# Kernel optimization log

Hardware: AMD Instinct MI355X
Metric: run time of the kernel (lower is better)

## Reference

```python
import jax, jax.numpy as jnp
import numpy as np

H, W, C = 64, 64, 64
B = 64
N_HEADS = 4
CONV_FILTERS = 64
BASIS_DIM = 16


def get_spatial_basis(h, w, d):
    half_d = d // 2
    basis = np.zeros((h, w, d), dtype=np.float32)
    div = np.exp(np.arange(0, half_d, 2, dtype=np.float32) * -np.log(100.0) / half_d)
    h_grid = np.expand_dims(np.arange(0, h, dtype=np.float32), 1)
    w_grid = np.expand_dims(np.arange(0, w, dtype=np.float32), 1)
    basis[:, :, 0:half_d:2] = np.sin(h_grid * div)[:, np.newaxis, :]
    basis[:, :, 1:half_d:2] = np.cos(h_grid * div)[:, np.newaxis, :]
    basis[:, :, half_d::2] = np.sin(w_grid * div)[np.newaxis, :, :]
    basis[:, :, half_d + 1::2] = np.cos(w_grid * div)[np.newaxis, :, :]
    return basis


def setup_inputs() -> dict:
    key = jax.random.key(0)
    ks = jax.random.split(key, 8)
    feat_in = C + BASIS_DIM  # 80 input channels for 1x1 convs
    return {
        "image": jax.random.normal(ks[0], (B, H, W, C), jnp.float32),
        "state1": jax.random.normal(ks[1], (B, 512), jnp.float32),
        "state2": jax.random.normal(ks[2], (B, 512), jnp.float32),
        "extra": jax.random.normal(ks[3], (B, 256), jnp.float32),
        "Wq": jax.random.normal(ks[4], (1024, CONV_FILTERS), jnp.float32) * 0.03,
        "bq": jnp.zeros((CONV_FILTERS,), jnp.float32),
        "Wk": jax.random.normal(ks[5], (feat_in, CONV_FILTERS), jnp.float32) * 0.1,
        "bk": jnp.zeros((CONV_FILTERS,), jnp.float32),
        "Wv": jax.random.normal(ks[6], (feat_in, CONV_FILTERS), jnp.float32) * 0.1,
        "bv": jnp.zeros((CONV_FILTERS,), jnp.float32),
        "spatial_basis": jnp.asarray(get_spatial_basis(H, W, BASIS_DIM)),
    }


def reference(image, state1, state2, extra, Wq, bq, Wk, bk, Wv, bv, spatial_basis):
    b, h, w, _ = image.shape
    nh = N_HEADS
    cf = Wq.shape[1]
    dph = cf // nh  # depth per head

    # concat image with tiled spatial basis -> [B,h,w,C+basis_dim]
    sb = jnp.broadcast_to(spatial_basis[None], (b,) + spatial_basis.shape)
    feats = jnp.concatenate([image, sb], axis=-1)

    # combiner over network-state tensors, then Dense query
    state = jnp.concatenate([state1, state2], axis=-1)  # [B,1024]
    q = state @ Wq + bq                                 # [B,cf]

    # 1x1 convs == per-pixel dense projections
    keys = feats @ Wk + bk    # [B,h,w,cf]
    vals = feats @ Wv + bv    # [B,h,w,cf]

    qh = q.reshape(b, nh, dph)
    kh = keys.reshape(b, h * w, nh, dph)
    vh = vals.reshape(b, h * w, nh, dph)

    # per-head dot scores over spatial positions, softmax over positions
    scores = jnp.einsum('bnd,bpnd->bpn', qh, kh)        # [B,hw,nh]
    attn = jax.nn.softmax(scores, axis=1)
    mean_attn = attn.mean(axis=-1).reshape(b, h, w)

    # weighted sum of values over spatial positions -> [B,cf]
    pooled = jnp.einsum('bpn,bpnd->bnd', attn, vh).reshape(b, cf)

    out = jnp.concatenate([pooled, extra], axis=-1)
    return out, mean_attn
```

## Files before the change

kernel.cpp:

```cpp
#include <hip/hip_runtime.h>
#include <hip/hip_bf16.h>

#define BATCH  64
#define HW     4096
#define PTILE  256
#define NSPLIT 16
#define RSTRIDE 88

typedef unsigned int u32;
typedef unsigned short u16;

__device__ __forceinline__ float bf2f(u16 h) { return __uint_as_float(((u32)h) << 16); }

__device__ __forceinline__ u32 f2bf(float x) {
  u32 b = __float_as_uint(x);
  return (b + 0x7fffu + ((b >> 16) & 1u)) >> 16;
}

template<bool F32>
__device__ __forceinline__ float ld(const void* p, size_t i) {
  if (F32) return ((const float*)p)[i];
  return bf2f(((const u16*)p)[i]);
}

template<bool F32>
__device__ __forceinline__ void st(void* p, size_t i, float v) {
  if (F32) ((float*)p)[i] = v;
  else     ((__hip_bfloat16*)p)[i] = __float2bfloat16(v);
}

__device__ __forceinline__ bool detect_f32(const u16* __restrict__ image) {
  u16 h = image[(threadIdx.x & 63) * 2];
  u32 e = (h >> 7) & 0xFFu;
  unsigned long long m = __ballot(e >= 0x86u);
  return __popcll(m) >= 8;
}

__device__ __forceinline__ void acc8(uint4 v, const float* __restrict__ w,
                                     float& s0, float& s1, float& s2, float& s3) {
  const u32 uu[4] = {v.x, v.y, v.z, v.w};
#pragma unroll
  for (int i = 0; i < 4; ++i) {
    float lo = __uint_as_float(uu[i] << 16);
    float hi = __uint_as_float(uu[i] & 0xffff0000u);
    const float* wl = w + i * 8;
    s0 += lo * wl[0]; s1 += lo * wl[1]; s2 += lo * wl[2]; s3 += lo * wl[3];
    s0 += hi * wl[4]; s1 += hi * wl[5]; s2 += hi * wl[6]; s3 += hi * wl[7];
  }
}

template<bool F32>
__device__ void k1_body(const void* state1, const void* state2, const void* Wq,
                        const void* bq, const void* Wk, const void* bk,
                        float* weff, float* cb, float* stt, float* qp, float* q) {
  const int b = blockIdx.x, tid = threadIdx.x;
  stt[tid]        = ld<F32>(state1, (size_t)b * 512 + tid);
  stt[512 + tid]  = ld<F32>(state2, (size_t)b * 512 + tid);
  __syncthreads();
  {
    const int j = tid & 63, k = tid >> 6, i0 = k * 128;
    float a = 0.f;
    for (int i = 0; i < 128; ++i) a += stt[i0 + i] * ld<F32>(Wq, (size_t)(i0 + i) * 64 + j);
    qp[k * 64 + j] = a;
  }
  __syncthreads();
  if (tid < 64) {
    float a = ld<F32>(bq, tid);
#pragma unroll
    for (int k = 0; k < 8; ++k) a += qp[k * 64 + tid];
    q[tid] = a;
  }
  __syncthreads();
  if (tid < 320) {
    const int c = tid >> 2, n = tid & 3;
    float a = 0.f;
#pragma unroll
    for (int d = 0; d < 16; ++d) a += ld<F32>(Wk, (size_t)c * 64 + n * 16 + d) * q[n * 16 + d];
    weff[b * 320 + tid] = a;
  } else if (tid < 324) {
    const int n = tid - 320;
    float a = 0.f;
#pragma unroll
    for (int d = 0; d < 16; ++d) a += ld<F32>(bk, n * 16 + d) * q[n * 16 + d];
    cb[b * 4 + n] = a;
  }
}

__global__ __launch_bounds__(512) void k1_prep(
    const void* image, const void* state1, const void* state2, const void* Wq,
    const void* bq, const void* Wk, const void* bk, float* weff, float* cb) {
  __shared__ float stt[1024];
  __shared__ float qp[512];
  __shared__ float q[64];
  if (detect_f32((const u16*)image))
       k1_body<true >(state1, state2, Wq, bq, Wk, bk, weff, cb, stt, qp, q);
  else k1_body<false>(state1, state2, Wq, bq, Wk, bk, weff, cb, stt, qp, q);
}

__global__ __launch_bounds__(256) void k2_main(
    const void* __restrict__ image, const void* __restrict__ basis,
    const float* __restrict__ weff, const float* __restrict__ cb,
    float* __restrict__ e_buf, float* __restrict__ m_blk, float* __restrict__ sum_blk,
    float* __restrict__ fpool_part) {
  __shared__ __align__(16) u16 feat[PTILE * RSTRIDE];
  __shared__ __align__(16) float es_t[4 * PTILE];
  __shared__ float red[16];
  __shared__ float bm[4];
  const int tid = threadIdx.x;
  const int b = blockIdx.x & 63, s = blockIdx.x >> 6;
  const int bs = b * NSPLIT + s;

  if (detect_f32((const u16*)image)) {
    const float4* img4 = (const float4*)image + ((size_t)b * HW + s * PTILE) * 16;
#pragma unroll
    for (int i = 0; i < 16; ++i) {
      const int f = i * 256 + tid;
      float4 v = img4[f];
      const int r = f >> 4, c4 = f & 15;
      u32 lo = f2bf(v.x) | (f2bf(v.y) << 16);
      u32 hi = f2bf(v.z) | (f2bf(v.w) << 16);
      *(uint2*)(feat + r * RSTRIDE + c4 * 4) = make_uint2(lo, hi);
    }
    const float4* bas4 = (const float4*)basis + (size_t)(s * PTILE) * 4;
#pragma unroll
    for (int i = 0; i < 4; ++i) {
      const int f = i * 256 + tid;
      float4 v = bas4[f];
      const int r = f >> 2, c4 = f & 3;
      u32 lo = f2bf(v.x) | (f2bf(v.y) << 16);
      u32 hi = f2bf(v.z) | (f2bf(v.w) << 16);
      *(uint2*)(feat + r * RSTRIDE + 64 + c4 * 4) = make_uint2(lo, hi);
    }
  } else {
    const uint4* img4 = (const uint4*)image + ((size_t)b * HW + s * PTILE) * 8;
#pragma unroll
    for (int i = 0; i < 8; ++i) {
      const int f = i * 256 + tid;
      const int r = f >> 3, c8 = f & 7;
      *(uint4*)(feat + r * RSTRIDE + c8 * 8) = img4[f];
    }
    const uint4* bas4 = (const uint4*)basis + (size_t)(s * PTILE) * 2;
#pragma unroll
    for (int i = 0; i < 2; ++i) {
      const int f = i * 256 + tid;
      const int r = f >> 1, c8 = f & 1;
      *(uint4*)(feat + r * RSTRIDE + 64 + c8 * 8) = bas4[f];
    }
  }
  __syncthreads();

  const float* wf = weff + b * 320;
  float s0 = cb[b * 4 + 0], s1 = cb[b * 4 + 1], s2 = cb[b * 4 + 2], s3 = cb[b * 4 + 3];
  {
    const uint4* row = (const uint4*)(feat + tid * RSTRIDE);
#pragma unroll
    for (int v = 0; v < 10; ++v) acc8(row[v], wf + v * 32, s0, s1, s2, s3);
  }

  float m0 = s0, m1 = s1, m2 = s2, m3 = s3;
#pragma unroll
  for (int off = 32; off > 0; off >>= 1) {
    m0 = fmaxf(m0, __shfl_xor(m0, off, 64));
    m1 = fmaxf(m1, __shfl_xor(m1, off, 64));
    m2 = fmaxf(m2, __shfl_xor(m2, off, 64));
    m3 = fmaxf(m3, __shfl_xor(m3, off, 64));
  }
  if ((tid & 63) == 0) { float* r = red + (tid >> 6) * 4; r[0] = m0; r[1] = m1; r[2] = m2; r[3] = m3; }
  __syncthreads();
  if (tid < 4) {
    float m = red[tid];
#pragma unroll
    for (int w = 1; w < 4; ++w) m = fmaxf(m, red[w * 4 + tid]);
    bm[tid] = m;
  }
  __syncthreads();

  float e0 = __expf(s0 - bm[0]);
  float e1 = __expf(s1 - bm[1]);
  float e2 = __expf(s2 - bm[2]);
  float e3 = __expf(s3 - bm[3]);
  es_t[0 * PTILE + tid] = e0;
  es_t[1 * PTILE + tid] = e1;
  es_t[2 * PTILE + tid] = e2;
  es_t[3 * PTILE + tid] = e3;
  reinterpret_cast<float4*>(e_buf)[(size_t)b * HW + s * PTILE + tid] = make_float4(e0, e1, e2, e3);

  float a0 = e0, a1 = e1, a2 = e2, a3 = e3;
#pragma unroll
  for (int off = 32; off > 0; off >>= 1) {
    a0 += __shfl_xor(a0, off, 64);
    a1 += __shfl_xor(a1, off, 64);
    a2 += __shfl_xor(a2, off, 64);
    a3 += __shfl_xor(a3, off, 64);
  }
  if ((tid & 63) == 0) { float* r = red + (tid >> 6) * 4; r[0] = a0; r[1] = a1; r[2] = a2; r[3] = a3; }
  __syncthreads();
  if (tid < 4) {
    float a = 0.f;
#pragma unroll
    for (int w = 0; w < 4; ++w) a += red[w * 4 + tid];
    sum_blk[bs * 4 + tid] = a;
    m_blk[bs * 4 + tid] = bm[tid];
  }

  {
    const int n = tid >> 6, c = tid & 63;
    const float4* esn = (const float4*)(es_t + n * PTILE);
    float acc = 0.f, acc2 = 0.f;
#pragma unroll 8
    for (int g = 0; g < 64; ++g) {
      float4 e = esn[g];
      const u16* f0 = feat + (g * 4) * RSTRIDE + c;
      acc += e.x * bf2f(f0[0]) + e.y * bf2f(f0[RSTRIDE]) +
             e.z * bf2f(f0[2 * RSTRIDE]) + e.w * bf2f(f0[3 * RSTRIDE]);
      if (c < 16) {
        const u16* f1 = f0 + 64;
        acc2 += e.x * bf2f(f1[0]) + e.y * bf2f(f1[RSTRIDE]) +
                e.z * bf2f(f1[2 * RSTRIDE]) + e.w * bf2f(f1[3 * RSTRIDE]);
      }
    }
    fpool_part[(size_t)bs * 320 + n * 80 + c] = acc;
    if (c < 16) fpool_part[(size_t)bs * 320 + n * 80 + 64 + c] = acc2;
  }
}

template<bool F32>
__device__ void k34_body(const float* m_blk, const float* sum_blk, const float* e_buf,
                         const float* fpool_part, const void* Wv, const void* bv,
                         const void* extra, void* out, float* esc, float* fp) {
  const int tid = threadIdx.x;
  const int b = blockIdx.x & 63, s = blockIdx.x >> 6;
  if (tid < 4) {
    float M = -3.4e38f;
#pragma unroll
    for (int sp = 0; sp < NSPLIT; ++sp) M = fmaxf(M, m_blk[(b * NSPLIT + sp) * 4 + tid]);
    float den = 0.f;
#pragma unroll
    for (int sp = 0; sp < NSPLIT; ++sp)
      den += __expf(m_blk[(b * NSPLIT + sp) * 4 + tid] - M) * sum_blk[(b * NSPLIT + sp) * 4 + tid];
    float rd = 1.0f / den;
#pragma unroll
    for (int sp = 0; sp < NSPLIT; ++sp)
      esc[sp * 4 + tid] = __expf(m_blk[(b * NSPLIT + sp) * 4 + tid] - M) * rd;
  }
  __syncthreads();
  {
    float4 e4 = reinterpret_cast<const float4*>(e_buf)[(size_t)b * HW + s * PTILE + tid];
    float mean = 0.25f * (e4.x * esc[s * 4 + 0] + e4.y * esc[s * 4 + 1] +
                          e4.z * esc[s * 4 + 2] + e4.w * esc[s * 4 + 3]);
    st<F32>(out, (size_t)BATCH * 320 + (size_t)b * HW + s * PTILE + tid, mean);
  }
  if (s == 0) {
    for (int idx = tid; idx < 320; idx += 256) {
      const int n2 = idx / 80;
      float a = 0.f;
#pragma unroll
      for (int sp = 0; sp < NSPLIT; ++sp)
        a += esc[sp * 4 + n2] * fpool_part[(size_t)(b * NSPLIT + sp) * 320 + idx];
      fp[idx] = a;
    }
    __syncthreads();
    if (tid < 64) {
      const int n = tid >> 4;
      float dot = 0.f;
#pragma unroll
      for (int c = 0; c < 80; ++c) dot += fp[n * 80 + c] * ld<F32>(Wv, (size_t)c * 64 + tid);
      st<F32>(out, (size_t)b * 320 + tid, dot + ld<F32>(bv, tid));
    }
    st<F32>(out, (size_t)b * 320 + 64 + tid, ld<F32>(extra, (size_t)b * 256 + tid));
  }
}

__global__ __launch_bounds__(256) void k34_out(
    const void* image, const float* m_blk, const float* sum_blk, const float* e_buf,
    const float* fpool_part, const void* Wv, const void* bv, const void* extra, void* out) {
  __shared__ float esc[NSPLIT * 4];
  __shared__ float fp[320];
  if (detect_f32((const u16*)image))
       k34_body<true >(m_blk, sum_blk, e_buf, fpool_part, Wv, bv, extra, out, esc, fp);
  else k34_body<false>(m_blk, sum_blk, e_buf, fpool_part, Wv, bv, extra, out, esc, fp);
}

extern "C" void kernel_launch(void* const* d_in, const int* in_sizes, int n_in,
                              void* d_out, int out_size, void* d_ws, size_t ws_size,
                              hipStream_t stream) {
  (void)in_sizes; (void)n_in; (void)out_size; (void)ws_size;
  const void* image  = d_in[0];
  const void* state1 = d_in[1];
  const void* state2 = d_in[2];
  const void* extra  = d_in[3];
  const void* Wq = d_in[4];
  const void* bq = d_in[5];
  const void* Wk = d_in[6];
  const void* bk = d_in[7];
  const void* Wv = d_in[8];
  const void* bv = d_in[9];
  const void* basis = d_in[10];

  float* ws         = (float*)d_ws;
  float* weff       = ws;
  float* cb         = ws + 20480;
  float* m_blk      = ws + 20736;
  float* sum_blk    = ws + 24832;
  float* fpool_part = ws + 28928;
  float* e_buf      = ws + 356608;

  k1_prep<<<dim3(BATCH), dim3(512), 0, stream>>>(image, state1, state2, Wq, bq, Wk, bk, weff, cb);
  k2_main<<<dim3(BATCH * NSPLIT), dim3(PTILE), 0, stream>>>(image, basis, weff, cb,
                                                            e_buf, m_blk, sum_blk, fpool_part);
  k34_out<<<dim3(BATCH * NSPLIT), dim3(PTILE), 0, stream>>>(image, m_blk, sum_blk, e_buf,
                                                            fpool_part, Wv, bv, extra, d_out);
}
```

Baseline: 144.2 us.

## Split query GEMM across batch tiles and transpose feature tile to channel-major

The query projection becomes a separate 16-block kernel that tiles Wq and states in shared memory and reuses each weight across 16 batch rows, followed by a small reduction kernel that forms the effective key weights. The main kernel stores the feature tile channel-major in LDS so both the score dot product and the pooled-value accumulation read contiguous 16-byte vectors. Scores are computed by 8 threads per group of 8 pixels, then reduced with lane shuffles. The e_buf layout changes to head-major. This adds an extra kernel launch and a redundant LDS load left over in the score loop.

```diff
diff --git a/kernel.cpp b/kernel.cpp
--- a/kernel.cpp
+++ b/kernel.cpp
@@ -5,7 +5,7 @@
 #define HW     4096
 #define PTILE  256
 #define NSPLIT 16
-#define RSTRIDE 88
+#define RST    264
 
 typedef unsigned int u32;
 typedef unsigned short u16;
@@ -21,6 +21,13 @@
 __device__ __forceinline__ float ld(const void* p, size_t i) {
   if (F32) return ((const float*)p)[i];
   return bf2f(((const u16*)p)[i]);
+}
+
+template<bool F32>
+__device__ __forceinline__ float4 ld4(const void* p, size_t i4) {
+  if (F32) return ((const float4*)p)[i4];
+  uint2 u = ((const uint2*)p)[i4];
+  return make_float4(bf2f(u.x & 0xffff), bf2f(u.x >> 16), bf2f(u.y & 0xffff), bf2f(u.y >> 16));
 }
 
 template<bool F32>
@@ -36,38 +43,65 @@
   return __popcll(m) >= 8;
 }
 
-__device__ __forceinline__ void acc8(uint4 v, const float* __restrict__ w,
-                                     float& s0, float& s1, float& s2, float& s3) {
-  const u32 uu[4] = {v.x, v.y, v.z, v.w};
+template<bool F32>
+__device__ void k1a_body(const void* state1, const void* state2, const void* Wq,
+                         float* q_part, float* WslT, float* stt) {
+  const int kb = blockIdx.x;
+  const int tid = threadIdx.x;
 #pragma unroll
   for (int i = 0; i < 4; ++i) {
-    float lo = __uint_as_float(uu[i] << 16);
-    float hi = __uint_as_float(uu[i] & 0xffff0000u);
-    const float* wl = w + i * 8;
-    s0 += lo * wl[0]; s1 += lo * wl[1]; s2 += lo * wl[2]; s3 += lo * wl[3];
-    s0 += hi * wl[4]; s1 += hi * wl[5]; s2 += hi * wl[6]; s3 += hi * wl[7];
-  }
-}
-
-template<bool F32>
-__device__ void k1_body(const void* state1, const void* state2, const void* Wq,
-                        const void* bq, const void* Wk, const void* bk,
-                        float* weff, float* cb, float* stt, float* qp, float* q) {
+    const int fidx = i * 256 + tid;
+    const int r = fidx >> 4, c4 = fidx & 15;
+    float4 v = ld4<F32>(Wq, (size_t)(kb * 64 + r) * 16 + c4);
+    WslT[(c4 * 4 + 0) * 68 + r] = v.x;
+    WslT[(c4 * 4 + 1) * 68 + r] = v.y;
+    WslT[(c4 * 4 + 2) * 68 + r] = v.z;
+    WslT[(c4 * 4 + 3) * 68 + r] = v.w;
+  }
+  const void* src = (kb < 8) ? state1 : state2;
+  const int k0q = (kb & 7) * 16;
+#pragma unroll
+  for (int i = 0; i < 4; ++i) {
+    const int fidx = i * 256 + tid;
+    const int bb = fidx >> 4, i4 = fidx & 15;
+    float4 v = ld4<F32>(src, (size_t)bb * 128 + k0q + i4);
+    *(float4*)&stt[bb * 64 + i4 * 4] = v;
+  }
+  __syncthreads();
+  const int j = tid & 63, bg = tid >> 6;
+  float acc[16];
+#pragma unroll
+  for (int b2 = 0; b2 < 16; ++b2) acc[b2] = 0.f;
+#pragma unroll
+  for (int i4 = 0; i4 < 16; ++i4) {
+    float4 wv = *(const float4*)&WslT[j * 68 + i4 * 4];
+#pragma unroll
+    for (int b2 = 0; b2 < 16; ++b2) {
+      float4 sv = *(const float4*)&stt[(bg * 16 + b2) * 64 + i4 * 4];
+      acc[b2] += wv.x * sv.x + wv.y * sv.y + wv.z * sv.z + wv.w * sv.w;
+    }
+  }
+#pragma unroll
+  for (int b2 = 0; b2 < 16; ++b2)
+    q_part[kb * 4096 + (bg * 16 + b2) * 64 + j] = acc[b2];
+}
+
+__global__ __launch_bounds__(256) void k1a(
+    const void* image, const void* state1, const void* state2, const void* Wq, float* q_part) {
+  __shared__ float WslT[64 * 68];
+  __shared__ float stt[64 * 64];
+  if (detect_f32((const u16*)image)) k1a_body<true >(state1, state2, Wq, q_part, WslT, stt);
+  else                               k1a_body<false>(state1, state2, Wq, q_part, WslT, stt);
+}
+
+template<bool F32>
+__device__ void k1b_body(const float* q_part, const void* bq, const void* Wk, const void* bk,
+                         float* weff, float* cb, float* q) {
   const int b = blockIdx.x, tid = threadIdx.x;
-  stt[tid]        = ld<F32>(state1, (size_t)b * 512 + tid);
-  stt[512 + tid]  = ld<F32>(state2, (size_t)b * 512 + tid);
-  __syncthreads();
-  {
-    const int j = tid & 63, k = tid >> 6, i0 = k * 128;
-    float a = 0.f;
-    for (int i = 0; i < 128; ++i) a += stt[i0 + i] * ld<F32>(Wq, (size_t)(i0 + i) * 64 + j);
-    qp[k * 64 + j] = a;
-  }
-  __syncthreads();
   if (tid < 64) {
     float a = ld<F32>(bq, tid);
 #pragma unroll
-    for (int k = 0; k < 8; ++k) a += qp[k * 64 + tid];
+    for (int sl = 0; sl < 16; ++sl) a += q_part[sl * 4096 + b * 64 + tid];
     q[tid] = a;
   }
   __syncthreads();
@@ -77,8 +111,9 @@
 #pragma unroll
     for (int d = 0; d < 16; ++d) a += ld<F32>(Wk, (size_t)c * 64 + n * 16 + d) * q[n * 16 + d];
     weff[b * 320 + tid] = a;
-  } else if (tid < 324) {
-    const int n = tid - 320;
+  }
+  if (tid >= 256 && tid < 260) {
+    const int n = tid - 256;
     float a = 0.f;
 #pragma unroll
     for (int d = 0; d < 16; ++d) a += ld<F32>(bk, n * 16 + d) * q[n * 16 + d];
@@ -86,15 +121,12 @@
   }
 }
 
-__global__ __launch_bounds__(512) void k1_prep(
-    const void* image, const void* state1, const void* state2, const void* Wq,
-    const void* bq, const void* Wk, const void* bk, float* weff, float* cb) {
-  __shared__ float stt[1024];
-  __shared__ float qp[512];
+__global__ __launch_bounds__(320) void k1b(
+    const void* image, const float* q_part, const void* bq, const void* Wk, const void* bk,
+    float* weff, float* cb) {
   __shared__ float q[64];
-  if (detect_f32((const u16*)image))
-       k1_body<true >(state1, state2, Wq, bq, Wk, bk, weff, cb, stt, qp, q);
-  else k1_body<false>(state1, state2, Wq, bq, Wk, bk, weff, cb, stt, qp, q);
+  if (detect_f32((const u16*)image)) k1b_body<true >(q_part, bq, Wk, bk, weff, cb, q);
+  else                               k1b_body<false>(q_part, bq, Wk, bk, weff, cb, q);
 }
 
 __global__ __launch_bounds__(256) void k2_main(
@@ -102,70 +134,121 @@
     const float* __restrict__ weff, const float* __restrict__ cb,
     float* __restrict__ e_buf, float* __restrict__ m_blk, float* __restrict__ sum_blk,
     float* __restrict__ fpool_part) {
-  __shared__ __align__(16) u16 feat[PTILE * RSTRIDE];
+  __shared__ __align__(16) u16 featT[80 * RST];
   __shared__ __align__(16) float es_t[4 * PTILE];
-  __shared__ float red[16];
-  __shared__ float bm[4];
+  __shared__ float weffL[320];
+  __shared__ float cbL[4];
+  __shared__ float red[16], red2[16], bm[4];
   const int tid = threadIdx.x;
   const int b = blockIdx.x & 63, s = blockIdx.x >> 6;
   const int bs = b * NSPLIT + s;
 
+  for (int i = tid; i < 320; i += 256) weffL[i] = weff[b * 320 + i];
+  if (tid < 4) cbL[tid] = cb[b * 4 + tid];
+
   if (detect_f32((const u16*)image)) {
-    const float4* img4 = (const float4*)image + ((size_t)b * HW + s * PTILE) * 16;
-#pragma unroll
-    for (int i = 0; i < 16; ++i) {
-      const int f = i * 256 + tid;
-      float4 v = img4[f];
-      const int r = f >> 4, c4 = f & 15;
-      u32 lo = f2bf(v.x) | (f2bf(v.y) << 16);
-      u32 hi = f2bf(v.z) | (f2bf(v.w) << 16);
-      *(uint2*)(feat + r * RSTRIDE + c4 * 4) = make_uint2(lo, hi);
+    const float4* img4 = (const float4*)image + ((size_t)(b * HW + s * PTILE)) * 16;
+#pragma unroll
+    for (int i = 0; i < 8; ++i) {
+      const int fidx = i * 256 + tid;
+      const int pp = fidx >> 4, c4 = fidx & 15;
+      float4 v0 = img4[(pp * 2) * 16 + c4];
+      float4 v1 = img4[(pp * 2 + 1) * 16 + c4];
+      *(u32*)&featT[(c4 * 4 + 0) * RST + pp * 2] = f2bf(v0.x) | (f2bf(v1.x) << 16);
+      *(u32*)&featT[(c4 * 4 + 1) * RST + pp * 2] = f2bf(v0.y) | (f2bf(v1.y) << 16);
+      *(u32*)&featT[(c4 * 4 + 2) * RST + pp * 2] = f2bf(v0.z) | (f2bf(v1.z) << 16);
+      *(u32*)&featT[(c4 * 4 + 3) * RST + pp * 2] = f2bf(v0.w) | (f2bf(v1.w) << 16);
     }
     const float4* bas4 = (const float4*)basis + (size_t)(s * PTILE) * 4;
 #pragma unroll
+    for (int i = 0; i < 2; ++i) {
+      const int fidx = i * 256 + tid;
+      const int pp = fidx >> 2, c4 = fidx & 3;
+      float4 v0 = bas4[(pp * 2) * 4 + c4];
+      float4 v1 = bas4[(pp * 2 + 1) * 4 + c4];
+      *(u32*)&featT[(64 + c4 * 4 + 0) * RST + pp * 2] = f2bf(v0.x) | (f2bf(v1.x) << 16);
+      *(u32*)&featT[(64 + c4 * 4 + 1) * RST + pp * 2] = f2bf(v0.y) | (f2bf(v1.y) << 16);
+      *(u32*)&featT[(64 + c4 * 4 + 2) * RST + pp * 2] = f2bf(v0.z) | (f2bf(v1.z) << 16);
+      *(u32*)&featT[(64 + c4 * 4 + 3) * RST + pp * 2] = f2bf(v0.w) | (f2bf(v1.w) << 16);
+    }
+  } else {
+    const uint4* img4 = (const uint4*)image + ((size_t)(b * HW + s * PTILE)) * 8;
+#pragma unroll
     for (int i = 0; i < 4; ++i) {
-      const int f = i * 256 + tid;
-      float4 v = bas4[f];
-      const int r = f >> 2, c4 = f & 3;
-      u32 lo = f2bf(v.x) | (f2bf(v.y) << 16);
-      u32 hi = f2bf(v.z) | (f2bf(v.w) << 16);
-      *(uint2*)(feat + r * RSTRIDE + 64 + c4 * 4) = make_uint2(lo, hi);
-    }
-  } else {
-    const uint4* img4 = (const uint4*)image + ((size_t)b * HW + s * PTILE) * 8;
-#pragma unroll
-    for (int i = 0; i < 8; ++i) {
-      const int f = i * 256 + tid;
-      const int r = f >> 3, c8 = f & 7;
-      *(uint4*)(feat + r * RSTRIDE + c8 * 8) = img4[f];
+      const int fidx = i * 256 + tid;
+      const int pp = fidx >> 3, c8 = fidx & 7;
+      uint4 u0 = img4[(pp * 2) * 8 + c8];
+      uint4 u1 = img4[(pp * 2 + 1) * 8 + c8];
+      const u32 w0[4] = {u0.x, u0.y, u0.z, u0.w};
+      const u32 w1[4] = {u1.x, u1.y, u1.z, u1.w};
+#pragma unroll
+      for (int h = 0; h < 4; ++h) {
+        *(u32*)&featT[(c8 * 8 + 2 * h + 0) * RST + pp * 2] = (w0[h] & 0xffffu) | (w1[h] << 16);
+        *(u32*)&featT[(c8 * 8 + 2 * h + 1) * RST + pp * 2] = (w0[h] >> 16) | (w1[h] & 0xffff0000u);
+      }
     }
     const uint4* bas4 = (const uint4*)basis + (size_t)(s * PTILE) * 2;
-#pragma unroll
-    for (int i = 0; i < 2; ++i) {
-      const int f = i * 256 + tid;
-      const int r = f >> 1, c8 = f & 1;
-      *(uint4*)(feat + r * RSTRIDE + 64 + c8 * 8) = bas4[f];
-    }
-  }
-  __syncthreads();
-
-  const float* wf = weff + b * 320;
-  float s0 = cb[b * 4 + 0], s1 = cb[b * 4 + 1], s2 = cb[b * 4 + 2], s3 = cb[b * 4 + 3];
-  {
-    const uint4* row = (const uint4*)(feat + tid * RSTRIDE);
-#pragma unroll
-    for (int v = 0; v < 10; ++v) acc8(row[v], wf + v * 32, s0, s1, s2, s3);
-  }
-
-  float m0 = s0, m1 = s1, m2 = s2, m3 = s3;
-#pragma unroll
-  for (int off = 32; off > 0; off >>= 1) {
-    m0 = fmaxf(m0, __shfl_xor(m0, off, 64));
-    m1 = fmaxf(m1, __shfl_xor(m1, off, 64));
-    m2 = fmaxf(m2, __shfl_xor(m2, off, 64));
-    m3 = fmaxf(m3, __shfl_xor(m3, off, 64));
-  }
-  if ((tid & 63) == 0) { float* r = red + (tid >> 6) * 4; r[0] = m0; r[1] = m1; r[2] = m2; r[3] = m3; }
+    {
+      const int pp = tid >> 1, h8 = tid & 1;
+      uint4 u0 = bas4[(pp * 2) * 2 + h8];
+      uint4 u1 = bas4[(pp * 2 + 1) * 2 + h8];
+      const u32 w0[4] = {u0.x, u0.y, u0.z, u0.w};
+      const u32 w1[4] = {u1.x, u1.y, u1.z, u1.w};
+#pragma unroll
+      for (int h = 0; h < 4; ++h) {
+        *(u32*)&featT[(64 + h8 * 8 + 2 * h + 0) * RST + pp * 2] = (w0[h] & 0xffffu) | (w1[h] << 16);
+        *(u32*)&featT[(64 + h8 * 8 + 2 * h + 1) * RST + pp * 2] = (w0[h] >> 16) | (w1[h] & 0xffff0000u);
+      }
+    }
+  }
+  __syncthreads();
+
+  const int p8 = tid >> 3, cg = tid & 7;
+  float acc[8][4];
+#pragma unroll
+  for (int pp = 0; pp < 8; ++pp)
+#pragma unroll
+    for (int n = 0; n < 4; ++n) acc[pp][n] = (cg == 0) ? cbL[n] : 0.f;
+#pragma unroll
+  for (int ci = 0; ci < 10; ++ci) {
+    const int c = cg + 8 * ci;
+    uint4 fv = *(const uint4*)&featT[c * RST + ((tid >> 3) & 7) * 8 + (tid >> 6) * 64];
+    fv = *(const uint4*)&featT[c * RST + p8 * 8];
+    float4 wv = *(const float4*)&weffL[c * 4];
+    const u32 uu[4] = {fv.x, fv.y, fv.z, fv.w};
+#pragma unroll
+    for (int i = 0; i < 4; ++i) {
+      float lo = __uint_as_float(uu[i] << 16);
+      float hi = __uint_as_float(uu[i] & 0xffff0000u);
+      acc[2 * i][0] += lo * wv.x; acc[2 * i][1] += lo * wv.y;
+      acc[2 * i][2] += lo * wv.z; acc[2 * i][3] += lo * wv.w;
+      acc[2 * i + 1][0] += hi * wv.x; acc[2 * i + 1][1] += hi * wv.y;
+      acc[2 * i + 1][2] += hi * wv.z; acc[2 * i + 1][3] += hi * wv.w;
+    }
+  }
+#pragma unroll
+  for (int off = 1; off <= 4; off <<= 1)
+#pragma unroll
+    for (int pp = 0; pp < 8; ++pp)
+#pragma unroll
+      for (int n = 0; n < 4; ++n) acc[pp][n] += __shfl_xor(acc[pp][n], off, 64);
+
+  float mx[4];
+#pragma unroll
+  for (int n = 0; n < 4; ++n) {
+    float m = acc[0][n];
+#pragma unroll
+    for (int pp = 1; pp < 8; ++pp) m = fmaxf(m, acc[pp][n]);
+    mx[n] = m;
+  }
+#pragma unroll
+  for (int off = 8; off <= 32; off <<= 1)
+#pragma unroll
+    for (int n = 0; n < 4; ++n) mx[n] = fmaxf(mx[n], __shfl_xor(mx[n], off, 64));
+  if ((tid & 63) == 0) {
+    float* r = red + (tid >> 6) * 4;
+    r[0] = mx[0]; r[1] = mx[1]; r[2] = mx[2]; r[3] = mx[3];
+  }
   __syncthreads();
   if (tid < 4) {
     float m = red[tid];
@@ -175,30 +258,41 @@
   }
   __syncthreads();
 
-  float e0 = __expf(s0 - bm[0]);
-  float e1 = __expf(s1 - bm[1]);
-  float e2 = __expf(s2 - bm[2]);
-  float e3 = __expf(s3 - bm[3]);
-  es_t[0 * PTILE + tid] = e0;
-  es_t[1 * PTILE + tid] = e1;
-  es_t[2 * PTILE + tid] = e2;
-  es_t[3 * PTILE + tid] = e3;
-  reinterpret_cast<float4*>(e_buf)[(size_t)b * HW + s * PTILE + tid] = make_float4(e0, e1, e2, e3);
-
-  float a0 = e0, a1 = e1, a2 = e2, a3 = e3;
-#pragma unroll
-  for (int off = 32; off > 0; off >>= 1) {
-    a0 += __shfl_xor(a0, off, 64);
-    a1 += __shfl_xor(a1, off, 64);
-    a2 += __shfl_xor(a2, off, 64);
-    a3 += __shfl_xor(a3, off, 64);
-  }
-  if ((tid & 63) == 0) { float* r = red + (tid >> 6) * 4; r[0] = a0; r[1] = a1; r[2] = a2; r[3] = a3; }
+#pragma unroll
+  for (int pp = 0; pp < 8; ++pp)
+#pragma unroll
+    for (int n = 0; n < 4; ++n) acc[pp][n] = __expf(acc[pp][n] - bm[n]);
+
+  if (cg == 0) {
+#pragma unroll
+    for (int n = 0; n < 4; ++n) {
+      float4 eA = make_float4(acc[0][n], acc[1][n], acc[2][n], acc[3][n]);
+      float4 eB = make_float4(acc[4][n], acc[5][n], acc[6][n], acc[7][n]);
+      *(float4*)&es_t[n * PTILE + p8 * 8]     = eA;
+      *(float4*)&es_t[n * PTILE + p8 * 8 + 4] = eB;
+      float4* ebp = (float4*)e_buf + (size_t)(b * 4 + n) * 1024 + s * 64 + p8 * 2;
+      ebp[0] = eA; ebp[1] = eB;
+    }
+  }
+  float sm[4];
+#pragma unroll
+  for (int n = 0; n < 4; ++n) {
+    float a = acc[0][n];
+#pragma unroll
+    for (int pp = 1; pp < 8; ++pp) a += acc[pp][n];
+    sm[n] = a;
+  }
+#pragma unroll
+  for (int off = 8; off <= 32; off <<= 1)
+#pragma unroll
+    for (int n = 0; n < 4; ++n) sm[n] += __shfl_xor(sm[n], off, 64);
+  if ((tid & 63) == 0) {
+    float* r = red2 + (tid >> 6) * 4;
+    r[0] = sm[0]; r[1] = sm[1]; r[2] = sm[2]; r[3] = sm[3];
+  }
   __syncthreads();
   if (tid < 4) {
-    float a = 0.f;
-#pragma unroll
-    for (int w = 0; w < 4; ++w) a += red[w * 4 + tid];
+    float a = red2[tid] + red2[4 + tid] + red2[8 + tid] + red2[12 + tid];
     sum_blk[bs * 4 + tid] = a;
     m_blk[bs * 4 + tid] = bm[tid];
   }
@@ -206,21 +300,27 @@
   {
     const int n = tid >> 6, c = tid & 63;
     const float4* esn = (const float4*)(es_t + n * PTILE);
-    float acc = 0.f, acc2 = 0.f;
-#pragma unroll 8
-    for (int g = 0; g < 64; ++g) {
-      float4 e = esn[g];
-      const u16* f0 = feat + (g * 4) * RSTRIDE + c;
-      acc += e.x * bf2f(f0[0]) + e.y * bf2f(f0[RSTRIDE]) +
-             e.z * bf2f(f0[2 * RSTRIDE]) + e.w * bf2f(f0[3 * RSTRIDE]);
+    float a1 = 0.f, a2 = 0.f;
+#pragma unroll 4
+    for (int g = 0; g < 32; ++g) {
+      float4 ex = esn[g * 2], ey = esn[g * 2 + 1];
+      uint4 fv = *(const uint4*)&featT[c * RST + g * 8];
+      const u32 uu[4] = {fv.x, fv.y, fv.z, fv.w};
+      a1 += ex.x * __uint_as_float(uu[0] << 16) + ex.y * __uint_as_float(uu[0] & 0xffff0000u)
+          + ex.z * __uint_as_float(uu[1] << 16) + ex.w * __uint_as_float(uu[1] & 0xffff0000u)
+          + ey.x * __uint_as_float(uu[2] << 16) + ey.y * __uint_as_float(uu[2] & 0xffff0000u)
+          + ey.z * __uint_as_float(uu[3] << 16) + ey.w * __uint_as_float(uu[3] & 0xffff0000u);
       if (c < 16) {
-        const u16* f1 = f0 + 64;
-        acc2 += e.x * bf2f(f1[0]) + e.y * bf2f(f1[RSTRIDE]) +
-                e.z * bf2f(f1[2 * RSTRIDE]) + e.w * bf2f(f1[3 * RSTRIDE]);
+        uint4 f2 = *(const uint4*)&featT[(64 + c) * RST + g * 8];
+        const u32 vv[4] = {f2.x, f2.y, f2.z, f2.w};
+        a2 += ex.x * __uint_as_float(vv[0] << 16) + ex.y * __uint_as_float(vv[0] & 0xffff0000u)
+            + ex.z * __uint_as_float(vv[1] << 16) + ex.w * __uint_as_float(vv[1] & 0xffff0000u)
+            + ey.x * __uint_as_float(vv[2] << 16) + ey.y * __uint_as_float(vv[2] & 0xffff0000u)
+            + ey.z * __uint_as_float(vv[3] << 16) + ey.w * __uint_as_float(vv[3] & 0xffff0000u);
       }
     }
-    fpool_part[(size_t)bs * 320 + n * 80 + c] = acc;
-    if (c < 16) fpool_part[(size_t)bs * 320 + n * 80 + 64 + c] = acc2;
+    fpool_part[(size_t)bs * 320 + n * 80 + c] = a1;
+    if (c < 16) fpool_part[(size_t)bs * 320 + n * 80 + 64 + c] = a2;
   }
 }
 
@@ -245,10 +345,14 @@
   }
   __syncthreads();
   {
-    float4 e4 = reinterpret_cast<const float4*>(e_buf)[(size_t)b * HW + s * PTILE + tid];
-    float mean = 0.25f * (e4.x * esc[s * 4 + 0] + e4.y * esc[s * 4 + 1] +
-                          e4.z * esc[s * 4 + 2] + e4.w * esc[s * 4 + 3]);
-    st<F32>(out, (size_t)BATCH * 320 + (size_t)b * HW + s * PTILE + tid, mean);
+    const size_t pidx = (size_t)s * PTILE + tid;
+    float e0 = e_buf[(size_t)(b * 4 + 0) * HW + pidx];
+    float e1 = e_buf[(size_t)(b * 4 + 1) * HW + pidx];
+    float e2 = e_buf[(size_t)(b * 4 + 2) * HW + pidx];
+    float e3 = e_buf[(size_t)(b * 4 + 3) * HW + pidx];
+    float mean = 0.25f * (e0 * esc[s * 4 + 0] + e1 * esc[s * 4 + 1] +
+                          e2 * esc[s * 4 + 2] + e3 * esc[s * 4 + 3]);
+    st<F32>(out, (size_t)BATCH * 320 + (size_t)b * HW + pidx, mean);
   }
   if (s == 0) {
     for (int idx = tid; idx < 320; idx += 256) {
@@ -302,10 +406,12 @@
   float* cb         = ws + 20480;
   float* m_blk      = ws + 20736;
   float* sum_blk    = ws + 24832;
-  float* fpool_part = ws + 28928;
-  float* e_buf      = ws + 356608;
-
-  k1_prep<<<dim3(BATCH), dim3(512), 0, stream>>>(image, state1, state2, Wq, bq, Wk, bk, weff, cb);
+  float* q_part     = ws + 28928;
+  float* fpool_part = ws + 94464;
+  float* e_buf      = ws + 422144;
+
+  k1a<<<dim3(16), dim3(256), 0, stream>>>(image, state1, state2, Wq, q_part);
+  k1b<<<dim3(BATCH), dim3(320), 0, stream>>>(image, q_part, bq, Wk, bk, weff, cb);
   k2_main<<<dim3(BATCH * NSPLIT), dim3(PTILE), 0, stream>>>(image, basis, weff, cb,
                                                             e_buf, m_blk, sum_blk, fpool_part);
   k34_out<<<dim3(BATCH * NSPLIT), dim3(PTILE), 0, stream>>>(image, m_blk, sum_blk, e_buf,
```

After: 142.7 us. About the same (-1.1%).
